# Kernel optimization log

Hardware: AMD Instinct MI355X
Metric: run time of the kernel (lower is better)

Reference implementation:

```python
import math
import jax, jax.numpy as jnp
import numpy as np

DIMS = 20
MULT = 8
K = (DIMS + 1) * MULT  # 168 mixture components
N = 524288
EPS = 1.0              # log_density default eps
BASE_COV = 0.1
LOG_NORM = -DIMS / 2 * math.log(2 * math.pi)


def setup_inputs() -> dict:
    key = jax.random.key(0)
    k1, k2, k3 = jax.random.split(key, 3)
    sample = jax.random.normal(k1, (N, DIMS), dtype=jnp.float32) * 0.3
    alpha = jax.random.normal(k2, (K,), dtype=jnp.float32) * 0.1
    mu = jax.random.uniform(k3, (K, DIMS), dtype=jnp.float32, minval=-0.5, maxval=0.5)
    cov = jnp.full((K, DIMS), BASE_COV, dtype=jnp.float32)
    return {"sample": sample, "alpha": alpha, "mu": mu, "cov": cov}


def reference(sample, alpha, mu, cov):
    # Faithful vectorization of the per-component Python loop in log_density.
    var = EPS ** 2
    weights = jax.nn.softmax(alpha)                       # [K]
    i = jnp.arange(K) // MULT                             # component group index, 0..DIMS
    d = jnp.arange(DIMS)
    # cov[:i] *= var  ->  scale first i dims of each component's cov by var
    scale = jnp.where(d[None, :] < i[:, None], var, 1.0)  # [K, D]
    inv = 1.0 / (cov * scale)                             # [K, D]
    # det_cov = var**i * (1/10)**(dims - i)  (exactly as in the source)
    fi = i.astype(jnp.float32)
    det_cov = var ** fi * BASE_COV ** (DIMS - fi)         # [K]
    sig_term = det_cov ** -0.5                            # [K]
    # quad[n,k] = sum_d (x[n,d]-mu[k,d])^2 * inv[k,d], expanded into GEMMs
    quad = (sample ** 2) @ inv.T \
           - 2.0 * (sample @ (mu * inv).T) \
           + jnp.sum(mu * mu * inv, axis=1)[None, :]      # [N, K]
    results = sig_term * jnp.exp(-0.5 * quad) * weights   # [N, K]
    density = results.sum(axis=1, keepdims=True)          # [N, 1]
    return jnp.log(density) + LOG_NORM
```

## Files before the change

### kernel.cpp

```cpp
#include <hip/hip_runtime.h>
#include <math.h>


#define DIMS     20
#define MULT     8
#define K_COMP   168
#define KC_PAD   176
#define NTILE    11
#define BASE_COV 0.1f
#define LOG2E    1.4426950408889634f
#define LN2      0.6931471805599453f
#define LOG_NORM -18.378770664093453f
#define CPW      4
#define NBLK     8192

typedef _Float16 f16x8 __attribute__((ext_vector_type(8)));
typedef _Float16 f16x2 __attribute__((ext_vector_type(2)));
typedef float    f32x4 __attribute__((ext_vector_type(4)));
typedef unsigned int uint;
typedef uint u32x4 __attribute__((ext_vector_type(4)));

__device__ __forceinline__ uint pk(float lo, float hi) {
    return __builtin_bit_cast(uint, __builtin_amdgcn_cvt_pkrtz(lo, hi));
}
__device__ __forceinline__ uint pksq(uint a) {
    f16x2 v = __builtin_bit_cast(f16x2, a);
    return __builtin_bit_cast(uint, (f16x2)(v * v));
}

__global__ void gm_precompute(const float* __restrict__ alpha,
                              const float* __restrict__ mu,
                              const float* __restrict__ cov,
                              uint4* __restrict__ tbl) {
    __shared__ _Float16 C[KC_PAD][64];
    __shared__ float sh_logZ;
    const int tid = threadIdx.x;

    uint* cz = (uint*)&C[0][0];
    for (int i = tid; i < KC_PAD * 64 / 2; i += 256) cz[i] = 0u;
    __syncthreads();

    if (tid < 64) {
        float a0 = (tid       < K_COMP) ? alpha[tid]       : -1e30f;
        float a1 = (tid + 64  < K_COMP) ? alpha[tid + 64]  : -1e30f;
        float a2 = (tid + 128 < K_COMP) ? alpha[tid + 128] : -1e30f;
        float m = fmaxf(fmaxf(a0, a1), a2);
        for (int msk = 32; msk; msk >>= 1) m = fmaxf(m, __shfl_xor(m, msk, 64));
        float s = __expf(a0 - m) + __expf(a1 - m) + __expf(a2 - m);
        for (int msk = 32; msk; msk >>= 1) s += __shfl_xor(s, msk, 64);
        if (tid == 0) sh_logZ = m + __logf(s);
    }
    __syncthreads();

    if (tid < K_COMP) {
        const int   n  = tid;
        const int   i  = n / MULT;
        const float fi = (float)i;
        const float var = 1.0f;
        float logdet = fi * __logf(var) + ((float)DIMS - fi) * __logf(BASE_COV);
        float Csum = 0.0f;
        for (int d = 0; d < DIMS; ++d) {
            float scale = (d < i) ? var : 1.0f;
            float inv   = 1.0f / (cov[n * DIMS + d] * scale);
            float mm    = mu[n * DIMS + d];
            Csum += mm * mm * inv;
            C[n][d]        = (_Float16)(-0.5f * inv * LOG2E);
            C[n][DIMS + d] = (_Float16)(mm * inv * LOG2E);
        }
        float L2 = ((alpha[n] - sh_logZ) - 0.5f * logdet - 0.5f * Csum) * LOG2E;
        C[n][2 * DIMS] = (_Float16)L2;
    } else if (tid < KC_PAD) {
        C[tid][2 * DIMS] = (_Float16)(-65504.0f);
    }
    __syncthreads();

    for (int e = tid; e < NTILE * 2 * 64; e += 256) {
        int t    = e >> 7;
        int h    = (e >> 6) & 1;
        int lane = e & 63;
        int q = lane >> 4, c = lane & 15;
        tbl[e] = *(const uint4*)&C[t * 16 + c][h * 32 + q * 8];
    }
}

__global__ __launch_bounds__(64, 3) void gm_density(const float* __restrict__ sample,
                                                    const f16x8* __restrict__ tbl,
                                                    float* __restrict__ out) {
    const int l = threadIdx.x;
    const int q = l >> 4, c = l & 15;
    const bool qa = (q & 1) != 0, qb = (q & 2) != 0;
    const uint onezero = 0x00003C00u;
    const f32x4 zero = { 0.f, 0.f, 0.f, 0.f };

#define LOAD_CF(T)                                                              \
    const f16x8 cf1_##T = tbl[(T) * 128 + l];                                   \
    const f16x8 cf2_##T = tbl[(T) * 128 + 64 + l];
    LOAD_CF(0) LOAD_CF(1) LOAD_CF(2) LOAD_CF(3) LOAD_CF(4) LOAD_CF(5)
    LOAD_CF(6) LOAD_CF(7) LOAD_CF(8) LOAD_CF(9) LOAD_CF(10)
#undef LOAD_CF

    const int base = blockIdx.x * (16 * CPW);

    const float4* rp0 = (const float4*)(sample + (size_t)(base + c) * DIMS);
    float4 r0 = rp0[0], r1 = rp0[1], r2 = rp0[2], r3 = rp0[3], r4 = rp0[4];

#define DO_TILE(T)                                                              \
        {                                                                       \
            f32x4 acc = __builtin_amdgcn_mfma_f32_16x16x32_f16(cf1_##T, sf1, zero, 0, 0, 0); \
            acc       = __builtin_amdgcn_mfma_f32_16x16x32_f16(cf2_##T, sf2, acc,  0, 0, 0); \
            p0 += __builtin_amdgcn_exp2f(acc[0]);                               \
            p1 += __builtin_amdgcn_exp2f(acc[1]);                               \
            p2 += __builtin_amdgcn_exp2f(acc[2]);                               \
            p3 += __builtin_amdgcn_exp2f(acc[3]);                               \
        }

#define DO_CHUNK(CC)                                                            \
    {                                                                           \
        uint q0 = pk(r0.x, r0.y), q1 = pk(r0.z, r0.w);                          \
        uint q2 = pk(r1.x, r1.y), q3 = pk(r1.z, r1.w);                          \
        uint q4 = pk(r2.x, r2.y), q5 = pk(r2.z, r2.w);                          \
        uint q6 = pk(r3.x, r3.y), q7 = pk(r3.z, r3.w);                          \
        uint q8 = pk(r4.x, r4.y), q9 = pk(r4.z, r4.w);                          \
         \
         \
        if ((CC) + 1 < CPW) {                                                   \
            uint dep = q9;                                                      \
            asm volatile("v_and_b32 %0, 0, %0" : "+v"(dep));                    \
            const float4* np = (const float4*)(sample                           \
                + (size_t)(base + ((CC) + 1) * 16 + c) * DIMS + dep);           \
            r0 = np[0]; r1 = np[1]; r2 = np[2]; r3 = np[3]; r4 = np[4];         \
        }                                                                       \
        uint s0 = pksq(q0), s1 = pksq(q1), s2 = pksq(q2), s3 = pksq(q3);        \
        uint s4 = pksq(q4), s5 = pksq(q5), s6 = pksq(q6), s7 = pksq(q7);        \
        uint s8 = pksq(q8), s9 = pksq(q9);                                      \
        uint f1_0 = qb ? (qa ? q2 : s8) : (qa ? s4 : s0);                       \
        uint f1_1 = qb ? (qa ? q3 : s9) : (qa ? s5 : s1);                       \
        uint f1_2 = qb ? (qa ? q4 : q0) : (qa ? s6 : s2);                       \
        uint f1_3 = qb ? (qa ? q5 : q1) : (qa ? s7 : s3);                       \
        uint f2_0 = qb ? 0u : (qa ? onezero : q6);                              \
        uint f2_1 = qb ? 0u : (qa ? 0u : q7);                                   \
        uint f2_2 = qb ? 0u : (qa ? 0u : q8);                                   \
        uint f2_3 = qb ? 0u : (qa ? 0u : q9);                                   \
        u32x4 w1 = { f1_0, f1_1, f1_2, f1_3 };                                  \
        u32x4 w2 = { f2_0, f2_1, f2_2, f2_3 };                                  \
        f16x8 sf1 = __builtin_bit_cast(f16x8, w1);                              \
        f16x8 sf2 = __builtin_bit_cast(f16x8, w2);                              \
        float p0 = 0.f, p1 = 0.f, p2 = 0.f, p3 = 0.f;       \
        DO_TILE(0) DO_TILE(1) DO_TILE(2) DO_TILE(3) DO_TILE(4) DO_TILE(5)       \
        DO_TILE(6) DO_TILE(7) DO_TILE(8) DO_TILE(9) DO_TILE(10)                 \
        float dens = (p0 + p1) + (p2 + p3);                                     \
        dens += __shfl_xor(dens, 16, 64);                                       \
        dens += __shfl_xor(dens, 32, 64);                                       \
        if (l < 16)                                                             \
            out[base + (CC) * 16 + l] = LN2 * __builtin_amdgcn_logf(dens) + LOG_NORM; \
    }

    DO_CHUNK(0) DO_CHUNK(1) DO_CHUNK(2) DO_CHUNK(3)
#undef DO_CHUNK
#undef DO_TILE
}

extern "C" void kernel_launch(void* const* d_in, const int* in_sizes, int n_in,
                              void* d_out, int out_size, void* d_ws, size_t ws_size,
                              hipStream_t stream) {
    const float* sample = (const float*)d_in[0];
    const float* alpha  = (const float*)d_in[1];
    const float* mu     = (const float*)d_in[2];
    const float* cov    = (const float*)d_in[3];
    float* out = (float*)d_out;
    uint4* tbl = (uint4*)d_ws;

    gm_precompute<<<1, 256, 0, stream>>>(alpha, mu, cov, tbl);
    gm_density<<<NBLK, 64, 0, stream>>>(sample, (const f16x8*)tbl, out);
}
```

Before: 97.06 us.

## Batch MFMA tiles before exp, drop manual prefetch, raise occupancy bound

Splits the 11 tiles into two groups. Each group issues all of its MFMAs first and then does the exp2 accumulations, so the exp work can hide MFMA latency. The explicit software prefetch of the next chunk's sample rows, with its fake dependency, is removed; each chunk now loads its own rows, leaving latency hiding to the scheduler and the extra occupancy. Launch bounds rise from 3 to 4 waves, which caps registers more tightly and risks spills given the 22 resident coefficient vectors.

```diff
diff --git a/kernel.cpp b/kernel.cpp
--- a/kernel.cpp
+++ b/kernel.cpp
@@ -83,7 +83,7 @@
     }
 }
 
-__global__ __launch_bounds__(64, 3) void gm_density(const float* __restrict__ sample,
+__global__ __launch_bounds__(64, 4) void gm_density(const float* __restrict__ sample,
                                                     const f16x8* __restrict__ tbl,
                                                     float* __restrict__ out) {
     const int l = threadIdx.x;
@@ -101,35 +101,24 @@
 
     const int base = blockIdx.x * (16 * CPW);
 
-    const float4* rp0 = (const float4*)(sample + (size_t)(base + c) * DIMS);
-    float4 r0 = rp0[0], r1 = rp0[1], r2 = rp0[2], r3 = rp0[3], r4 = rp0[4];
-
-#define DO_TILE(T)                                                              \
-        {                                                                       \
-            f32x4 acc = __builtin_amdgcn_mfma_f32_16x16x32_f16(cf1_##T, sf1, zero, 0, 0, 0); \
-            acc       = __builtin_amdgcn_mfma_f32_16x16x32_f16(cf2_##T, sf2, acc,  0, 0, 0); \
-            p0 += __builtin_amdgcn_exp2f(acc[0]);                               \
-            p1 += __builtin_amdgcn_exp2f(acc[1]);                               \
-            p2 += __builtin_amdgcn_exp2f(acc[2]);                               \
-            p3 += __builtin_amdgcn_exp2f(acc[3]);                               \
-        }
+#define TILE_ACC(T, ACC)                                                        \
+        f32x4 ACC = __builtin_amdgcn_mfma_f32_16x16x32_f16(cf1_##T, sf1, zero, 0, 0, 0); \
+        ACC       = __builtin_amdgcn_mfma_f32_16x16x32_f16(cf2_##T, sf2, ACC,  0, 0, 0);
+#define EXP_ACC(ACC)                                                            \
+        p0 += __builtin_amdgcn_exp2f(ACC[0]);                                   \
+        p1 += __builtin_amdgcn_exp2f(ACC[1]);                                   \
+        p2 += __builtin_amdgcn_exp2f(ACC[2]);                                   \
+        p3 += __builtin_amdgcn_exp2f(ACC[3]);
 
 #define DO_CHUNK(CC)                                                            \
     {                                                                           \
+        const float4* rp = (const float4*)(sample + (size_t)(base + (CC) * 16 + c) * DIMS); \
+        float4 r0 = rp[0], r1 = rp[1], r2 = rp[2], r3 = rp[3], r4 = rp[4];      \
         uint q0 = pk(r0.x, r0.y), q1 = pk(r0.z, r0.w);                          \
         uint q2 = pk(r1.x, r1.y), q3 = pk(r1.z, r1.w);                          \
         uint q4 = pk(r2.x, r2.y), q5 = pk(r2.z, r2.w);                          \
         uint q6 = pk(r3.x, r3.y), q7 = pk(r3.z, r3.w);                          \
         uint q8 = pk(r4.x, r4.y), q9 = pk(r4.z, r4.w);                          \
-         \
-         \
-        if ((CC) + 1 < CPW) {                                                   \
-            uint dep = q9;                                                      \
-            asm volatile("v_and_b32 %0, 0, %0" : "+v"(dep));                    \
-            const float4* np = (const float4*)(sample                           \
-                + (size_t)(base + ((CC) + 1) * 16 + c) * DIMS + dep);           \
-            r0 = np[0]; r1 = np[1]; r2 = np[2]; r3 = np[3]; r4 = np[4];         \
-        }                                                                       \
         uint s0 = pksq(q0), s1 = pksq(q1), s2 = pksq(q2), s3 = pksq(q3);        \
         uint s4 = pksq(q4), s5 = pksq(q5), s6 = pksq(q6), s7 = pksq(q7);        \
         uint s8 = pksq(q8), s9 = pksq(q9);                                      \
@@ -145,9 +134,17 @@
         u32x4 w2 = { f2_0, f2_1, f2_2, f2_3 };                                  \
         f16x8 sf1 = __builtin_bit_cast(f16x8, w1);                              \
         f16x8 sf2 = __builtin_bit_cast(f16x8, w2);                              \
-        float p0 = 0.f, p1 = 0.f, p2 = 0.f, p3 = 0.f;       \
-        DO_TILE(0) DO_TILE(1) DO_TILE(2) DO_TILE(3) DO_TILE(4) DO_TILE(5)       \
-        DO_TILE(6) DO_TILE(7) DO_TILE(8) DO_TILE(9) DO_TILE(10)                 \
+        float p0 = 0.f, p1 = 0.f, p2 = 0.f, p3 = 0.f;                           \
+                   \
+        { TILE_ACC(0, a0) TILE_ACC(1, a1) TILE_ACC(2, a2)                       \
+          TILE_ACC(3, a3) TILE_ACC(4, a4) TILE_ACC(5, a5)                       \
+          EXP_ACC(a0) EXP_ACC(a1) EXP_ACC(a2)                                   \
+          EXP_ACC(a3) EXP_ACC(a4) EXP_ACC(a5) }                                 \
+                           \
+        { TILE_ACC(6, b0) TILE_ACC(7, b1) TILE_ACC(8, b2)                       \
+          TILE_ACC(9, b3) TILE_ACC(10, b4)                                      \
+          EXP_ACC(b0) EXP_ACC(b1) EXP_ACC(b2)                                   \
+          EXP_ACC(b3) EXP_ACC(b4) }                                             \
         float dens = (p0 + p1) + (p2 + p3);                                     \
         dens += __shfl_xor(dens, 16, 64);                                       \
         dens += __shfl_xor(dens, 32, 64);                                       \
@@ -157,7 +154,8 @@
 
     DO_CHUNK(0) DO_CHUNK(1) DO_CHUNK(2) DO_CHUNK(3)
 #undef DO_CHUNK
-#undef DO_TILE
+#undef TILE_ACC
+#undef EXP_ACC
 }
 
 extern "C" void kernel_launch(void* const* d_in, const int* in_sizes, int n_in,
```

Measured after the change: 98.63 us. Within noise of the previous version (+1.6%).
